# Kernel optimization log

Measured on AMD Instinct MI355X. Metric: run time of the kernel, lower is better.

## Reference

```python
import jax, jax.numpy as jnp
import numpy as np
import math

B, S, H = 4, 1024, 1024
E, TOP_K, WINDOW = 4, 2, 64
CONFIGS = [(8, 'standard'), (12, 'standard'), (8, 'linear'), (8, 'local')]
PARAM_NAMES = ['Wq', 'bq', 'Wk', 'bk', 'Wv', 'bv', 'Wo', 'bo']


def setup_inputs() -> dict:
    key = jax.random.key(0)
    ks = jax.random.split(key, 2 + 8 * E)
    d = {}
    d['x'] = jax.random.normal(ks[0], (B, S, H), jnp.float32)
    d['Wg'] = jax.random.normal(ks[1], (H, E), jnp.float32) * 0.02
    i = 2
    for e, (nh, _) in enumerate(CONFIGS):
        hd = H // nh
        pd = nh * hd  # 1020 for nh=12, else 1024
        shapes = [(H, pd), (pd,), (H, pd), (pd,), (H, pd), (pd,), (pd, H), (H,)]
        for nm, shp in zip(PARAM_NAMES, shapes):
            d[f'e{e}_{nm}'] = jax.random.normal(ks[i], shp, jnp.float32) * 0.02
            i += 1
    d['attention_mask'] = jnp.ones((B, S), jnp.int32)
    return d


def _heads(y, nh, hd):
    b, s, _ = y.shape
    return y.reshape(b, s, nh, hd).transpose(0, 2, 1, 3)  # [b, nh, s, hd]


def _attention_expert(x, mask, Wq, bq, Wk, bk, Wv, bv, Wo, bo, nh, atype):
    b, s, _ = x.shape
    hd = Wq.shape[1] // nh
    scale = math.sqrt(hd)
    q = _heads(x @ Wq + bq, nh, hd)
    k = _heads(x @ Wk + bk, nh, hd)
    v = _heads(x @ Wv + bv, nh, hd)
    if atype == 'linear':
        # kernel-trick linear attention; original ignores attention_mask here
        q = jax.nn.elu(q) + 1.0
        k = jax.nn.elu(k) + 1.0
        kv = jnp.einsum('bhsd,bhse->bhde', k, v)
        num = jnp.einsum('bhqd,bhde->bhqe', q, kv)
        den = jnp.einsum('bhqd,bhd->bhq', q, k.sum(axis=2)) + 1e-6
        out = num / den[..., None]
    else:
        scores = jnp.einsum('bhqd,bhkd->bhqk', q, k) / scale
        if atype == 'local':
            idx = jnp.arange(s)
            dist = idx[None, :] - idx[:, None]  # j - i
            local_mask = jnp.abs(dist) <= WINDOW // 2
            scores = jnp.where(local_mask[None, None], scores, -jnp.inf)
        scores = jnp.where(mask[:, None, None, :] == 0, -jnp.inf, scores)
        probs = jax.nn.softmax(scores, axis=-1)
        probs = jnp.where(jnp.isnan(probs), 0.0, probs)  # nan_to_num(nan=0)
        out = jnp.einsum('bhqk,bhkd->bhqd', probs, v)
    out = out.transpose(0, 2, 1, 3).reshape(b, s, -1)
    return out @ Wo + bo


def _forward(x, Wg, eparams, attention_mask):
    b, s, h = x.shape
    # TopKGating (eval mode: no noise). logits -> top_k -> softmax over selected
    logits = x.reshape(-1, h) @ Wg  # [b*s, E]
    top_vals, top_idx = jax.lax.top_k(logits, TOP_K)
    gate_w = jax.nn.softmax(top_vals, axis=-1).reshape(b, s, TOP_K)
    sel = top_idx.reshape(b, s, TOP_K)
    outs = jnp.stack([
        _attention_expert(x, attention_mask, *eparams[e], CONFIGS[e][0], CONFIGS[e][1])
        for e in range(E)
    ], axis=0)  # [E, b, s, h]
    perm = outs.transpose(1, 2, 0, 3)  # [b, s, E, h]
    selected = jnp.take_along_axis(perm, sel[..., None], axis=2)  # [b, s, K, h]
    return (selected * gate_w[..., None]).sum(axis=2)


def reference(x, Wg,
              e0_Wq, e0_bq, e0_Wk, e0_bk, e0_Wv, e0_bv, e0_Wo, e0_bo,
              e1_Wq, e1_bq, e1_Wk, e1_bk, e1_Wv, e1_bv, e1_Wo, e1_bo,
              e2_Wq, e2_bq, e2_Wk, e2_bk, e2_Wv, e2_bv, e2_Wo, e2_bo,
              e3_Wq, e3_bq, e3_Wk, e3_bk, e3_Wv, e3_bv, e3_Wo, e3_bo,
              attention_mask):
    eparams = [
        (e0_Wq, e0_bq, e0_Wk, e0_bk, e0_Wv, e0_bv, e0_Wo, e0_bo),
        (e1_Wq, e1_bq, e1_Wk, e1_bk, e1_Wv, e1_bv, e1_Wo, e1_bo),
        (e2_Wq, e2_bq, e2_Wk, e2_bk, e2_Wv, e2_bv, e2_Wo, e2_bo),
        (e3_Wq, e3_bq, e3_Wk, e3_bk, e3_Wv, e3_bv, e3_Wo, e3_bo),
    ]
    return _forward(x, Wg, eparams, attention_mask)
```

## Files before the change

kernel.cpp:

```cpp
#include <hip/hip_runtime.h>
#include <cmath>

#define B_ 4
#define S_ 1024
#define H_ 1024

typedef short bf16x8 __attribute__((ext_vector_type(8)));
typedef float f32x4 __attribute__((ext_vector_type(4)));
typedef _Float16 half4 __attribute__((ext_vector_type(4)));

__device__ __forceinline__ unsigned short f2bf(float f) {
  unsigned u = __float_as_uint(f);
  u += 0x7fff + ((u >> 16) & 1);
  return (unsigned short)(u >> 16);
}
__device__ __forceinline__ float bf2f(unsigned short h) {
  return __uint_as_float(((unsigned)h) << 16);
}
__device__ __forceinline__ void gld16(const void* g, void* l) {
  __builtin_amdgcn_global_load_lds(
      (const __attribute__((address_space(1))) unsigned int*)g,
      (__attribute__((address_space(3))) unsigned int*)l, 16, 0, 0);
}

__global__ __launch_bounds__(64) void gate_kernel(
    const float* __restrict__ x, const float* __restrict__ Wg,
    float* __restrict__ gw) {
  int t = blockIdx.x;
  int lane = threadIdx.x;
  const float* xr = x + (size_t)t * H_;
  float a0 = 0.f, a1 = 0.f, a2 = 0.f, a3 = 0.f;
  for (int h = lane; h < H_; h += 64) {
    float xv = xr[h];
    const float* wr = Wg + h * 4;
    a0 += xv * wr[0]; a1 += xv * wr[1]; a2 += xv * wr[2]; a3 += xv * wr[3];
  }
  for (int off = 32; off > 0; off >>= 1) {
    a0 += __shfl_down(a0, off);
    a1 += __shfl_down(a1, off);
    a2 += __shfl_down(a2, off);
    a3 += __shfl_down(a3, off);
  }
  if (lane == 0) {
    float v[4] = {a0, a1, a2, a3};
    int i0 = 0; float b0 = v[0];
    for (int e = 1; e < 4; ++e) if (v[e] > b0) { b0 = v[e]; i0 = e; }
    int i1 = -1; float b1 = -INFINITY;
    for (int e = 0; e < 4; ++e) { if (e == i0) continue; if (v[e] > b1) { b1 = v[e]; i1 = e; } }
    float e1v = expf(b1 - b0);
    float w0 = 1.f / (1.f + e1v);
    float w1 = e1v / (1.f + e1v);
    float o[4] = {0.f, 0.f, 0.f, 0.f};
    o[i0] = w0; o[i1] = w1;
    float* g = gw + t * 4;
    g[0] = o[0]; g[1] = o[1]; g[2] = o[2]; g[3] = o[3];
  }
}

__global__ __launch_bounds__(64) void gate_conv_kernel(
    const float* __restrict__ x, const float* __restrict__ Wg,
    float* __restrict__ gw, unsigned short* __restrict__ xb) {
  int t = blockIdx.x;
  int lane = threadIdx.x;
  const float* xr = x + (size_t)t * H_;
  unsigned short* xbr = xb + (size_t)t * H_;
  float a0 = 0.f, a1 = 0.f, a2 = 0.f, a3 = 0.f;
  for (int h = lane; h < H_; h += 64) {
    float xv = xr[h];
    xbr[h] = f2bf(xv);
    const float* wr = Wg + h * 4;
    a0 += xv * wr[0]; a1 += xv * wr[1]; a2 += xv * wr[2]; a3 += xv * wr[3];
  }
  for (int off = 32; off > 0; off >>= 1) {
    a0 += __shfl_down(a0, off);
    a1 += __shfl_down(a1, off);
    a2 += __shfl_down(a2, off);
    a3 += __shfl_down(a3, off);
  }
  if (lane == 0) {
    float v[4] = {a0, a1, a2, a3};
    int i0 = 0; float b0 = v[0];
    for (int e = 1; e < 4; ++e) if (v[e] > b0) { b0 = v[e]; i0 = e; }
    int i1 = -1; float b1 = -INFINITY;
    for (int e = 0; e < 4; ++e) { if (e == i0) continue; if (v[e] > b1) { b1 = v[e]; i1 = e; } }
    float e1v = expf(b1 - b0);
    float w0 = 1.f / (1.f + e1v);
    float w1 = e1v / (1.f + e1v);
    float o[4] = {0.f, 0.f, 0.f, 0.f};
    o[i0] = w0; o[i1] = w1;
    float* g = gw + t * 4;
    g[0] = o[0]; g[1] = o[1]; g[2] = o[2]; g[3] = o[3];
  }
}

__global__ __launch_bounds__(256) void conv_kernel(
    const float* __restrict__ src, unsigned short* __restrict__ dst,
    int nsrc, int ldsrc) {
  int idx = blockIdx.x * 256 + threadIdx.x;
  int m = idx >> 10, c = idx & 1023;
  dst[idx] = (c < nsrc) ? f2bf(src[(size_t)m * ldsrc + c]) : (unsigned short)0;
}

__global__ __launch_bounds__(256) void wtrans4_kernel(
    const float* __restrict__ s0, const float* __restrict__ s1,
    const float* __restrict__ s2, const float* __restrict__ s3,
    unsigned short* __restrict__ d0, unsigned short* __restrict__ d1,
    unsigned short* __restrict__ d2, unsigned short* __restrict__ d3, int pd) {
  __shared__ float tile[32][33];
  int z = blockIdx.z;
  const float* src = (z == 0) ? s0 : (z == 1) ? s1 : (z == 2) ? s2 : s3;
  unsigned short* dst = (z == 0) ? d0 : (z == 1) ? d1 : (z == 2) ? d2 : d3;
  int ksrc = (z < 3) ? 1024 : pd;
  int nsrc = (z < 3) ? pd : 1024;
  int ldsrc = (z < 3) ? pd : 1024;
  int k0 = blockIdx.x * 32, n0 = blockIdx.y * 32;
  int tx = threadIdx.x & 31, ty = threadIdx.x >> 5;
  for (int i = 0; i < 32; i += 8) {
    int k = k0 + ty + i, n = n0 + tx;
    tile[ty + i][tx] = (k < ksrc && n < nsrc) ? src[(size_t)k * ldsrc + n] : 0.f;
  }
  __syncthreads();
  for (int i = 0; i < 32; i += 8) {
    int n = n0 + ty + i, k = k0 + tx;
    dst[(size_t)n * 1024 + k] = f2bf(tile[tx][ty + i]);
  }
}

struct W16 {
  const float* src[16];
  unsigned short* dst[16];
  int pd[4];
};
__global__ __launch_bounds__(256) void wtrans16_kernel(W16 p) {
  __shared__ float tile[32][33];
  int z = blockIdx.z;
  int e = z >> 2, m = z & 3;
  const float* src = p.src[z];
  unsigned short* dst = p.dst[z];
  int pd = p.pd[e];
  int ksrc = (m < 3) ? 1024 : pd;
  int nsrc = (m < 3) ? pd : 1024;
  int ldsrc = (m < 3) ? pd : 1024;
  int k0 = blockIdx.x * 32, n0 = blockIdx.y * 32;
  int tx = threadIdx.x & 31, ty = threadIdx.x >> 5;
  for (int i = 0; i < 32; i += 8) {
    int k = k0 + ty + i, n = n0 + tx;
    tile[ty + i][tx] = (k < ksrc && n < nsrc) ? src[(size_t)k * ldsrc + n] : 0.f;
  }
  __syncthreads();
  for (int i = 0; i < 32; i += 8) {
    int n = n0 + ty + i, k = k0 + tx;
    dst[(size_t)n * 1024 + k] = f2bf(tile[tx][ty + i]);
  }
}

__global__ __launch_bounds__(256) void gemm_mfma(
    const unsigned short* __restrict__ A, const unsigned short* __restrict__ Bt,
    const float* __restrict__ b0, const float* __restrict__ b1,
    const float* __restrict__ b2, void* __restrict__ Cv, int ldc,
    int nact, int elu_ncut, int out_bf16, int mode,
    const float* __restrict__ gw, int expert, int remap,
    int qs_ncut, float qscale) {
  constexpr int K = 1024;
  __shared__ __align__(16) unsigned short As[128 * 32];
  __shared__ __align__(16) unsigned short Bs[128 * 32];
  int tid = threadIdx.x, wave = tid >> 6, lane = tid & 63;
  int quad = lane >> 4, lrow = lane & 15;
  int rw = (wave >> 1) * 64, cw = (wave & 1) * 64;
  int m0 = blockIdx.y * 128, n0 = blockIdx.x * 128;
  int srow = wave * 32 + (lane >> 2);
  int scol = (lane & 3) * 8;
  const unsigned short* gA = A + (size_t)(m0 + srow) * K + scol;
  const unsigned short* gB = Bt + (size_t)(n0 + srow) * K + scol;
  unsigned short* lA = &As[wave * 1024];
  unsigned short* lB = &Bs[wave * 1024];
  f32x4 acc[4][4];
#pragma unroll
  for (int mt = 0; mt < 4; ++mt)
#pragma unroll
    for (int nt = 0; nt < 4; ++nt) acc[mt][nt] = (f32x4){0.f, 0.f, 0.f, 0.f};

  for (int k0 = 0; k0 < K; k0 += 32) {
    gld16(gA + k0, lA);
    gld16(gA + 16 * K + k0, lA + 512);
    gld16(gB + k0, lB);
    gld16(gB + 16 * K + k0, lB + 512);
    __syncthreads();
    bf16x8 af[4], bfr[4];
#pragma unroll
    for (int t = 0; t < 4; ++t) {
      af[t]  = *(const bf16x8*)&As[(rw + t * 16 + lrow) * 32 + quad * 8];
      bfr[t] = *(const bf16x8*)&Bs[(cw + t * 16 + lrow) * 32 + quad * 8];
    }
#pragma unroll
    for (int mt = 0; mt < 4; ++mt)
#pragma unroll
      for (int nt = 0; nt < 4; ++nt)
        acc[mt][nt] = __builtin_amdgcn_mfma_f32_16x16x32_bf16(
            af[mt], bfr[nt], acc[mt][nt], 0, 0, 0);
    __syncthreads();
  }
#pragma unroll
  for (int nt = 0; nt < 4; ++nt) {
    int n = n0 + cw + nt * 16 + lrow;
    int slice = n >> 10, noff = n & 1023;
    if (noff >= nact) continue;
    const float* bp = (slice == 0) ? b0 : (slice == 1) ? b1 : b2;
    float bias = bp[noff];
    bool do_elu = n < elu_ncut;
    bool do_qs = n < qs_ncut;
    int col = n;
    if (remap) {
      int head = (noff * 12337) >> 20;
      col = slice * 1152 + head * 96 + (noff - head * 85);
    }
#pragma unroll
    for (int mt = 0; mt < 4; ++mt) {
      int mb = m0 + rw + mt * 16 + quad * 4;
#pragma unroll
      for (int r = 0; r < 4; ++r) {
        int m = mb + r;
        float val = acc[mt][nt][r] + bias;
        if (do_elu) val = (val > 0.f) ? val + 1.f : expf(val);
        if (do_qs) val *= qscale;
        size_t ci = (size_t)m * ldc + col;
        if (out_bf16) {
          ((unsigned short*)Cv)[ci] = f2bf(val);
        } else {
          float* C = (float*)Cv;
          if (mode == 0) C[ci] = val;
          else {
            float g = gw[m * 4 + expert];
            if (mode == 1) C[ci] = g * val;
            else           C[ci] += g * val;
          }
        }
      }
    }
  }
}

__device__ __forceinline__ void stage_half(
    const unsigned short* __restrict__ G, int grow0, int kbase,
    unsigned short* lhalf, int wave, int lane) {
#pragma unroll
  for (int j = 0; j < 2; ++j) {
    int t = j * 512 + wave * 64 + lane;
    int rl = t >> 3;
    int cs = (t & 7) * 8;
    int c0 = cs ^ (((rl >> 2) & 1) << 4);
    gld16(G + (size_t)(grow0 + rl) * 1024 + kbase + c0,
          lhalf + (size_t)(j * 512 + wave * 64) * 8);
  }
}

__device__ __forceinline__ void gemm256_core(
    const unsigned short* __restrict__ A, const unsigned short* __restrict__ Bt,
    int m0, int n0, unsigned short* As, unsigned short* Bs,
    f32x4 (&acc)[8][4]) {
  int tid = threadIdx.x;
  int wave = tid >> 6, lane = tid & 63;
  int quad = lane >> 4, l15 = lane & 15;
  int wr = wave >> 2, wc = wave & 3;
#pragma unroll
  for (int mr = 0; mr < 8; ++mr)
#pragma unroll
    for (int nr = 0; nr < 4; ++nr) acc[mr][nr] = (f32x4){0.f, 0.f, 0.f, 0.f};
  stage_half(A, m0, 0, As, wave, lane);
  stage_half(A, m0 + 128, 0, As + 8192, wave, lane);
  stage_half(Bt, n0, 0, Bs, wave, lane);
  stage_half(Bt, n0 + 128, 0, Bs + 8192, wave, lane);
  __syncthreads();
  int cur = 0;
  for (int t = 0; t < 16; ++t) {
    const unsigned short* Ar = As + cur * 16384;
    const unsigned short* Br = Bs + cur * 16384;
    unsigned short* Awr = As + (cur ^ 1) * 16384;
    unsigned short* Bwr = Bs + (cur ^ 1) * 16384;
    int kb = (t + 1) * 64;
    bool more = (t + 1 < 16);
    bf16x8 bfr[4];
#pragma unroll
    for (int p = 0; p < 4; ++p) {
      const int ks = p >> 1, mh = (p & 1) * 4;
      bf16x8 af[4];
#pragma unroll
      for (int i = 0; i < 4; ++i) {
        int row = wr * 128 + (mh + i) * 16 + l15;
        int c = ks * 32 + quad * 8;
        af[i] = *(const bf16x8*)&Ar[row * 64 + (c ^ (((row >> 2) & 1) << 4))];
      }
      if ((p & 1) == 0) {
#pragma unroll
        for (int i = 0; i < 4; ++i) {
          int row = wc * 64 + i * 16 + l15;
          int c = ks * 32 + quad * 8;
          bfr[i] = *(const bf16x8*)&Br[row * 64 + (c ^ (((row >> 2) & 1) << 4))];
        }
      }
      if (more) {
        if (p == 0) stage_half(A, m0, kb, Awr, wave, lane);
        else if (p == 1) stage_half(A, m0 + 128, kb, Awr + 8192, wave, lane);
        else if (p == 2) stage_half(Bt, n0, kb, Bwr, wave, lane);
        else stage_half(Bt, n0 + 128, kb, Bwr + 8192, wave, lane);
      }
      __builtin_amdgcn_s_barrier();
      __builtin_amdgcn_s_setprio(1);
#pragma unroll
      for (int i = 0; i < 4; ++i)
#pragma unroll
        for (int jn = 0; jn < 4; ++jn)
          acc[mh + i][jn] = __builtin_amdgcn_mfma_f32_16x16x32_bf16(
              af[i], bfr[jn], acc[mh + i][jn], 0, 0, 0);
      __builtin_amdgcn_s_setprio(0);
      __builtin_amdgcn_s_barrier();
    }
    __syncthreads();
    cur ^= 1;
  }
}

struct QkvP {
  const unsigned short* Bt[4];
  const float* bq[4];
  const float* bk[4];
  const float* bv[4];
  unsigned short* C[4];
  int ldc[4];
  int nact[4];
  int elu_ncut[4];
  int remap[4];
  int qs_ncut[4];
  float qscale[4];
};
__global__ __launch_bounds__(512, 1) void gemm_qkv4_v2(
    const unsigned short* __restrict__ A, QkvP p) {
  __shared__ __align__(16) unsigned short As[2 * 256 * 64];
  __shared__ __align__(16) unsigned short Bs[2 * 256 * 64];
  int e = blockIdx.z;
  int flat = blockIdx.y * 12 + blockIdx.x;
  int swz = (flat & 7) * 24 + (flat >> 3);
  int m0 = (swz / 12) * 256, n0 = (swz % 12) * 256;
  f32x4 acc[8][4];
  gemm256_core(A, p.Bt[e], m0, n0, As, Bs, acc);
  int nact = p.nact[e], elu_ncut = p.elu_ncut[e], remap = p.remap[e];
  int qs_ncut = p.qs_ncut[e], ldc = p.ldc[e];
  float qscale = p.qscale[e];
  unsigned short* Cv = p.C[e];
  int tid = threadIdx.x, wave = tid >> 6, lane = tid & 63;
  int quad = lane >> 4, l15 = lane & 15;
  int wr = wave >> 2, wc = wave & 3;
#pragma unroll
  for (int nr = 0; nr < 4; ++nr) {
    int n = n0 + wc * 64 + nr * 16 + l15;
    int slice = n >> 10, noff = n & 1023;
    if (noff >= nact) continue;
    const float* bp = (slice == 0) ? p.bq[e] : (slice == 1) ? p.bk[e] : p.bv[e];
    float bias = bp[noff];
    bool do_elu = n < elu_ncut;
    bool do_qs = n < qs_ncut;
    int col = n;
    if (remap) {
      int head = (noff * 12337) >> 20;
      col = slice * 1152 + head * 96 + (noff - head * 85);
    }
#pragma unroll
    for (int mr = 0; mr < 8; ++mr) {
      int mb = m0 + wr * 128 + mr * 16 + quad * 4;
#pragma unroll
      for (int r = 0; r < 4; ++r) {
        int m = mb + r;
        float val = acc[mr][nr][r] + bias;
        if (do_elu) val = (val > 0.f) ? val + 1.f : expf(val);
        if (do_qs) val *= qscale;
        Cv[(size_t)m * ldc + col] = f2bf(val);
      }
    }
  }
}

struct OutP {
  const unsigned short* A[4];
  const unsigned short* B[4];
  const float* bias[4];
};
__global__ __launch_bounds__(512, 1) void gemm_out4_v2(
    OutP p, const float* __restrict__ gw, float* __restrict__ part) {
  __shared__ __align__(16) unsigned short As[2 * 256 * 64];
  __shared__ __align__(16) unsigned short Bs[2 * 256 * 64];
  int e = blockIdx.z;
  int flat = blockIdx.y * 4 + blockIdx.x;
  int swz = (flat & 7) * 8 + (flat >> 3);
  int m0 = (swz / 4) * 256, n0 = (swz % 4) * 256;
  f32x4 acc[8][4];
  gemm256_core(p.A[e], p.B[e], m0, n0, As, Bs, acc);
  const float* bp = p.bias[e];
  float* C = part + (size_t)e * (4096ull * 1024ull);
  int tid = threadIdx.x, wave = tid >> 6, lane = tid & 63;
  int quad = lane >> 4, l15 = lane & 15;
  int wr = wave >> 2, wc = wave & 3;
#pragma unroll
  for (int nr = 0; nr < 4; ++nr) {
    int n = n0 + wc * 64 + nr * 16 + l15;
    float bias = bp[n];
#pragma unroll
    for (int mr = 0; mr < 8; ++mr) {
      int mb = m0 + wr * 128 + mr * 16 + quad * 4;
#pragma unroll
      for (int r = 0; r < 4; ++r) {
        int m = mb + r;
        float g = gw[m * 4 + e];
        C[(size_t)m * 1024 + n] = g * (acc[mr][nr][r] + bias);
      }
    }
  }
}

__global__ __launch_bounds__(256) void reduce4(
    const float* __restrict__ part, float* __restrict__ out) {
  constexpr size_t N = 4096ull * 1024ull;
  size_t idx = ((size_t)blockIdx.x * 256 + threadIdx.x) * 4;
  f32x4 a0 = *(const f32x4*)(part + idx);
  f32x4 a1 = *(const f32x4*)(part + idx + N);
  f32x4 a2 = *(const f32x4*)(part + idx + 2 * N);
  f32x4 a3 = *(const f32x4*)(part + idx + 3 * N);
  f32x4 s;
#pragma unroll
  for (int j = 0; j < 4; ++j) {
    float t = a0[j];
    t += a1[j]; t += a2[j]; t += a3[j];
    s[j] = t;
  }
  *(f32x4*)(out + idx) = s;
}

__global__ __launch_bounds__(256) void padzero(
    unsigned short* __restrict__ qkv1, unsigned short* __restrict__ aob1) {
  int idx = blockIdx.x * 256 + threadIdx.x;
  int m = idx / 396, r = idx % 396;
  int slice = r / 132, r2 = r % 132;
  int head = r2 / 11, c = 85 + r2 % 11;
  qkv1[(size_t)m * 3456 + slice * 1152 + head * 96 + c] = 0;
  if (idx < 4096 * 4) {
    int mm = idx >> 2, cc = 1020 + (idx & 3);
    aob1[(size_t)mm * 1024 + cc] = 0;
  }
}

template <int HD, bool LOCAL>
__device__ __forceinline__ void attn_body(
    char* smem,
    const unsigned short* __restrict__ q, const unsigned short* __restrict__ k,
    const unsigned short* __restrict__ v, const int* __restrict__ amask,
    unsigned short* __restrict__ ao, int ldq, int h) {
  constexpr int HDP = (HD + 31) & ~31;
  constexpr int DCH = HDP / 32;
  constexpr int NDT = HDP / 16;
  constexpr int NCH = HDP / 8;
  constexpr int QT = 256, KT = 64;
  constexpr int KLD = HDP + 8;
  constexpr int VLD = KT + 4;
  constexpr int W2 = 32;
  constexpr int KSZ = KT * KLD;
  constexpr int VSZ = HDP * VLD;
  unsigned short* Ks = (unsigned short*)smem;
  _Float16* Vt = (_Float16*)(smem + 2 * KSZ * 2);
  unsigned long long* amq =
      (unsigned long long*)(smem + 2 * KSZ * 2 + 2 * VSZ * 2);
  int tid = threadIdx.x, wave = tid >> 6, lane = tid & 63;
  int quad = lane >> 4, l15 = lane & 15;
  int q0 = blockIdx.x * QT, b = blockIdx.z;
  size_t baseq = ((size_t)b * S_) * ldq + (size_t)h * HDP;
  size_t baseo = ((size_t)b * S_) * H_ + (size_t)h * HD;

  {
    unsigned long long bb0 = __ballot(amask[b * S_ + wave * 128 + lane] != 0);
    unsigned long long bb1 = __ballot(amask[b * S_ + wave * 128 + 64 + lane] != 0);
    if (lane == 0) { amq[wave * 2] = bb0; amq[wave * 2 + 1] = bb1; }
  }

  int qrow[2];
  bf16x8 qf[2][DCH];
#pragma unroll
  for (int g = 0; g < 2; ++g) {
    qrow[g] = q0 + wave * 32 + g * 16 + l15;
#pragma unroll
    for (int c = 0; c < DCH; ++c)
#pragma unroll
      for (int j = 0; j < 8; ++j) {
        int d = c * 32 + quad * 8 + j;
        qf[g][c][j] =
            (d < HD) ? (short)q[baseq + (size_t)qrow[g] * ldq + d] : (short)0;
      }
  }

  int jlo = 0, jhi = S_;
  if (LOCAL) {
    jlo = q0 - W2; if (jlo < 0) jlo = 0; jlo &= ~(KT - 1);
    jhi = q0 + QT + W2; if (jhi > S_) jhi = S_;
  }

  int skey = tid & 63, sc8a = tid >> 6, sc8b = 8 + (tid >> 6);
  bool sactb = sc8b < NCH;
  const unsigned short* kg = k + baseq + (size_t)skey * ldq;
  const unsigned short* vg = v + baseq + (size_t)skey * ldq;
  bf16x8 kra = {}, krb = {}, vra = {}, vrb = {};
  {
    size_t o = (size_t)jlo * ldq;
    kra = *(const bf16x8*)(kg + o + sc8a * 8);
    vra = *(const bf16x8*)(vg + o + sc8a * 8);
    if (sactb) {
      krb = *(const bf16x8*)(kg + o + sc8b * 8);
      vrb = *(const bf16x8*)(vg + o + sc8b * 8);
    }
  }

  {
    *(bf16x8*)&Ks[skey * KLD + sc8a * 8] = kra;
#pragma unroll
    for (int j = 0; j < 8; ++j)
      Vt[(sc8a * 8 + j) * VLD + skey] = (_Float16)bf2f((unsigned short)vra[j]);
    if (sactb) {
      *(bf16x8*)&Ks[skey * KLD + sc8b * 8] = krb;
#pragma unroll
      for (int j = 0; j < 8; ++j)
        Vt[(sc8b * 8 + j) * VLD + skey] = (_Float16)bf2f((unsigned short)vrb[j]);
    }
  }
  int cur = 0;
  __syncthreads();

  float m_run[2] = {-1e30f, -1e30f}, l_run[2] = {0.f, 0.f};
  f32x4 accd[2][NDT];
#pragma unroll
  for (int g = 0; g < 2; ++g)
#pragma unroll
    for (int dt = 0; dt < NDT; ++dt) accd[g][dt] = (f32x4){0.f, 0.f, 0.f, 0.f};

  for (int j0 = jlo; j0 < jhi; j0 += KT) {
    int jn = j0 + KT;
    if (jn < jhi) {
      size_t o = (size_t)jn * ldq;
      kra = *(const bf16x8*)(kg + o + sc8a * 8);
      vra = *(const bf16x8*)(vg + o + sc8a * 8);
      if (sactb) {
        krb = *(const bf16x8*)(kg + o + sc8b * 8);
        vrb = *(const bf16x8*)(vg + o + sc8b * 8);
      }
    }
    const unsigned short* KsR = Ks + cur * KSZ;
    const _Float16* VtR = Vt + cur * VSZ;
    f32x4 sf[2][4];
#pragma unroll
    for (int kt = 0; kt < 4; ++kt) {
      sf[0][kt] = (f32x4){0.f, 0.f, 0.f, 0.f};
      sf[1][kt] = (f32x4){0.f, 0.f, 0.f, 0.f};
#pragma unroll
      for (int c = 0; c < DCH; ++c) {
        bf16x8 kf = *(const bf16x8*)&KsR[(kt * 16 + l15) * KLD + c * 32 + quad * 8];
        sf[0][kt] = __builtin_amdgcn_mfma_f32_16x16x32_bf16(kf, qf[0][c], sf[0][kt], 0, 0, 0);
        sf[1][kt] = __builtin_amdgcn_mfma_f32_16x16x32_bf16(kf, qf[1][c], sf[1][kt], 0, 0, 0);
      }
    }
    unsigned long long mb = amq[j0 >> 6];
    unsigned mw[2] = {(unsigned)mb, (unsigned)(mb >> 32)};
    float pvv[2][4][4];
    float mx[2] = {-1e30f, -1e30f};
#pragma unroll
    for (int kt = 0; kt < 4; ++kt) {
      unsigned word = mw[kt >> 1];
      int sh = (kt & 1) * 16 + quad * 4;
#pragma unroll
      for (int r = 0; r < 4; ++r) {
        bool okm = (word >> (sh + r)) & 1;
#pragma unroll
        for (int g = 0; g < 2; ++g) {
          bool ok = okm;
          if (LOCAL) {
            int dj = (j0 + kt * 16 + quad * 4 + r) - qrow[g];
            ok = ok && (dj <= W2) && (dj >= -W2);
          }
          float s = ok ? sf[g][kt][r] : -1e30f;
          pvv[g][kt][r] = s;
          mx[g] = fmaxf(mx[g], s);
        }
      }
    }
    half4 pf[2][4];
    float aR[2][4];
#pragma unroll
    for (int g = 0; g < 2; ++g) {
      float mxg = fmaxf(mx[g], __shfl_xor(mx[g], 16));
      mxg = fmaxf(mxg, __shfl_xor(mxg, 32));
      float m_new = fmaxf(m_run[g], mxg);
      float psum = 0.f;
#pragma unroll
      for (int kt = 0; kt < 4; ++kt)
#pragma unroll
        for (int r = 0; r < 4; ++r) {
          float s = pvv[g][kt][r];
          float p = (s > -1e29f) ? __builtin_amdgcn_exp2f(s - m_new) : 0.f;
          pvv[g][kt][r] = p;
          psum += p;
        }
      psum += __shfl_xor(psum, 16);
      psum += __shfl_xor(psum, 32);
      float alpha = __builtin_amdgcn_exp2f(m_run[g] - m_new);
      m_run[g] = m_new;
      l_run[g] = l_run[g] * alpha + psum;
#pragma unroll
      for (int r = 0; r < 4; ++r)
        aR[g][r] = __shfl(alpha, (lane & 48) | (quad * 4 + r));
#pragma unroll
      for (int dt = 0; dt < NDT; ++dt)
#pragma unroll
        for (int r = 0; r < 4; ++r) accd[g][dt][r] *= aR[g][r];
#pragma unroll
      for (int kt = 0; kt < 4; ++kt)
#pragma unroll
        for (int r = 0; r < 4; ++r) pf[g][kt][r] = (_Float16)pvv[g][kt][r];
    }
    if (jn < jhi) {
      unsigned short* KsW = Ks + (cur ^ 1) * KSZ;
      _Float16* VtW = Vt + (cur ^ 1) * VSZ;
      *(bf16x8*)&KsW[skey * KLD + sc8a * 8] = kra;
#pragma unroll
      for (int j = 0; j < 8; ++j)
        VtW[(sc8a * 8 + j) * VLD + skey] = (_Float16)bf2f((unsigned short)vra[j]);
      if (sactb) {
        *(bf16x8*)&KsW[skey * KLD + sc8b * 8] = krb;
#pragma unroll
        for (int j = 0; j < 8; ++j)
          VtW[(sc8b * 8 + j) * VLD + skey] = (_Float16)bf2f((unsigned short)vrb[j]);
      }
    }
#pragma unroll
    for (int dt = 0; dt < NDT; ++dt)
#pragma unroll
      for (int kt = 0; kt < 4; ++kt) {
        half4 vf = *(const half4*)&VtR[(dt * 16 + l15) * VLD + kt * 16 + quad * 4];
        accd[0][dt] = __builtin_amdgcn_mfma_f32_16x16x16f16(pf[0][kt], vf, accd[0][dt], 0, 0, 0);
        accd[1][dt] = __builtin_amdgcn_mfma_f32_16x16x16f16(pf[1][kt], vf, accd[1][dt], 0, 0, 0);
      }
    __syncthreads();
    cur ^= 1;
  }
#pragma unroll
  for (int g = 0; g < 2; ++g) {
    float linv = (l_run[g] > 0.f) ? 1.f / l_run[g] : 0.f;
    float lR[4];
#pragma unroll
    for (int r = 0; r < 4; ++r)
      lR[r] = __shfl(linv, (lane & 48) | (quad * 4 + r));
#pragma unroll
    for (int dt = 0; dt < NDT; ++dt) {
      int d = dt * 16 + l15;
      if (d >= HD) continue;
#pragma unroll
      for (int r = 0; r < 4; ++r) {
        int row = q0 + wave * 32 + g * 16 + quad * 4 + r;
        ao[baseo + (size_t)row * H_ + d] = f2bf(accd[g][dt][r] * lR[r]);
      }
    }
  }
}

template <int HD, bool LOCAL>
__global__ __launch_bounds__(512) void attn_mfma3(
    const unsigned short* __restrict__ q, const unsigned short* __restrict__ k,
    const unsigned short* __restrict__ v, const int* __restrict__ amask,
    unsigned short* __restrict__ ao, int ldq) {
  constexpr int HDP = (HD + 31) & ~31;
  __shared__ __align__(16) char smem[2 * 64 * (HDP + 8) * 2 + 2 * HDP * 68 * 2 + 128];
  attn_body<HD, LOCAL>(smem, q, k, v, amask, ao, ldq, blockIdx.y);
}

#define NSPLIT 4
__device__ __forceinline__ void linkv_body(
    char* smemi, const unsigned short* __restrict__ k,
    const unsigned short* __restrict__ v, float* __restrict__ kvp,
    float* __restrict__ ksump, int ld, int h, int b, int split, int tid) {
  constexpr int HD = 128;
  constexpr int TLD = 34;
  unsigned short* Kt = (unsigned short*)smemi;
  unsigned short* Vt = Kt + HD * TLD;
  int bh = b * 8 + h;
  int wave = tid >> 6, lane = tid & 63;
  int quad = lane >> 4, l15 = lane & 15;
  int rw = (wave >> 1) * 64, cw = (wave & 1) * 64;
  size_t base = ((size_t)b * S_) * ld + (size_t)h * HD;
  int s_begin = split * (S_ / NSPLIT);

  f32x4 acc[4][4];
#pragma unroll
  for (int mt = 0; mt < 4; ++mt)
#pragma unroll
    for (int nt = 0; nt < 4; ++nt) acc[mt][nt] = (f32x4){0.f, 0.f, 0.f, 0.f};
  float ksacc = 0.f;
  int myd = tid & 127, half = tid >> 7;

  for (int c0 = 0; c0 < S_ / NSPLIT; c0 += 32) {
    for (int idx = tid; idx < 32 * HD; idx += 256) {
      int d = idx & 127, s = idx >> 7;
      size_t g = base + (size_t)(s_begin + c0 + s) * ld + d;
      Kt[d * TLD + s] = k[g];
      Vt[d * TLD + s] = v[g];
    }
    __syncthreads();
    bf16x8 af[4], bf[4];
#pragma unroll
    for (int t = 0; t < 4; ++t) {
      af[t] = *(const bf16x8*)&Vt[(rw + t * 16 + l15) * TLD + quad * 8];
      bf[t] = *(const bf16x8*)&Kt[(cw + t * 16 + l15) * TLD + quad * 8];
    }
#pragma unroll
    for (int mt = 0; mt < 4; ++mt)
#pragma unroll
      for (int nt = 0; nt < 4; ++nt)
        acc[mt][nt] = __builtin_amdgcn_mfma_f32_16x16x32_bf16(
            af[mt], bf[nt], acc[mt][nt], 0, 0, 0);
#pragma unroll
    for (int s = 0; s < 16; ++s)
      ksacc += bf2f(Kt[myd * TLD + half * 16 + s]);
    __syncthreads();
  }
  float* red = (float*)Kt;
  if (half == 1) red[myd] = ksacc;
  __syncthreads();
  if (half == 0)
    ksump[((size_t)split * 32 + bh) * HD + myd] = ksacc + red[myd];
  float* kvo = kvp + ((size_t)split * 32 + bh) * (HD * HD);
#pragma unroll
  for (int mt = 0; mt < 4; ++mt)
#pragma unroll
    for (int nt = 0; nt < 4; ++nt) {
      int dk = cw + nt * 16 + l15;
#pragma unroll
      for (int r = 0; r < 4; ++r) {
        int dv = rw + mt * 16 + quad * 4 + r;
        kvo[(size_t)dv * HD + dk] = acc[mt][nt][r];
      }
    }
}

__global__ __launch_bounds__(256) void linkv_mfma(
    const unsigned short* __restrict__ k, const unsigned short* __restrict__ v,
    float* __restrict__ kvp, float* __restrict__ ksump, int ld) {
  __shared__ __align__(16) char smemi[17408];
  linkv_body(smemi, k, v, kvp, ksump, ld, blockIdx.x, blockIdx.y, blockIdx.z,
             threadIdx.x);
}

__global__ __launch_bounds__(512) void attn_mega(
    const unsigned short* __restrict__ qkv0,
    const unsigned short* __restrict__ qkv1,
    const unsigned short* __restrict__ qkv2,
    const unsigned short* __restrict__ qkv3, const int* __restrict__ amask,
    unsigned short* __restrict__ ao0, unsigned short* __restrict__ ao1,
    unsigned short* __restrict__ ao3,
    float* __restrict__ kvp, float* __restrict__ ksump) {
  __shared__ __align__(16) char smem[69760];
  int y = blockIdx.y;
  if (y < 8)
    attn_body<128, false>(smem, qkv0, qkv0 + 1024, qkv0 + 2048, amask, ao0,
                          3072, y);
  else if (y < 20)
    attn_body<85, false>(smem, qkv1, qkv1 + 1152, qkv1 + 2304, amask, ao1,
                         3456, y - 8);
  else if (y < 28)
    attn_body<128, true>(smem, qkv3, qkv3 + 1024, qkv3 + 2048, amask, ao3,
                         3072, y - 20);
  else {
    int sub = threadIdx.x >> 8, stid = threadIdx.x & 255;
    int idx = (y - 28) * 8 + blockIdx.x * 2 + sub;
    linkv_body(smem + sub * 17408, qkv2 + 1024, qkv2 + 2048, kvp, ksump, 3072,
               idx & 7, blockIdx.z, idx >> 3, stid);
  }
}

__global__ __launch_bounds__(256) void linkv_reduce(
    const float* __restrict__ kvp, const float* __restrict__ ksump,
    unsigned short* __restrict__ kvb, float* __restrict__ ksum) {
  int idx = blockIdx.x * 256 + threadIdx.x;
  float s = 0.f;
#pragma unroll
  for (int p = 0; p < NSPLIT; ++p) s += kvp[(size_t)p * (32 * 128 * 128) + idx];
  kvb[idx] = f2bf(s);
  if (idx < 32 * 128) {
    float t = 0.f;
#pragma unroll
    for (int p = 0; p < NSPLIT; ++p) t += ksump[(size_t)p * (32 * 128) + idx];
    ksum[idx] = t;
  }
}

__global__ __launch_bounds__(256) void linattn_mfma(
    const unsigned short* __restrict__ q, const unsigned short* __restrict__ kvT,
    const float* __restrict__ ksum, unsigned short* __restrict__ ao, int ldq) {
  constexpr int KLD = 136;
  __shared__ __align__(16) unsigned short Ks[128 * KLD];
  __shared__ float ksL[128];
  int tid = threadIdx.x, wave = tid >> 6, lane = tid & 63;
  int quad = lane >> 4, l15 = lane & 15;
  int rw = (wave >> 1) * 64, cw = (wave & 1) * 64;
  int q0 = blockIdx.x * 128, h = blockIdx.y, b = blockIdx.z;
  int bh = b * 8 + h;
  size_t baseq = ((size_t)b * S_) * ldq + (size_t)h * 128;
  size_t baseo = ((size_t)b * S_) * H_ + (size_t)h * 128;
  const unsigned short* kvg = kvT + (size_t)bh * (128 * 128);
  for (int idx = tid; idx < 128 * 16; idx += 256) {
    int e = idx >> 4, c = idx & 15;
    *(bf16x8*)&Ks[e * KLD + c * 8] = *(const bf16x8*)&kvg[e * 128 + c * 8];
  }
  if (tid < 128) ksL[tid] = ksum[(size_t)bh * 128 + tid];
  bf16x8 qf[4][4];
#pragma unroll
  for (int mt = 0; mt < 4; ++mt) {
    const unsigned short* qr = q + baseq + (size_t)(q0 + rw + mt * 16 + l15) * ldq;
#pragma unroll
    for (int kc = 0; kc < 4; ++kc)
      qf[mt][kc] = *(const bf16x8*)&qr[kc * 32 + quad * 8];
  }
  __syncthreads();
  f32x4 acc[4][4];
#pragma unroll
  for (int mt = 0; mt < 4; ++mt)
#pragma unroll
    for (int nt = 0; nt < 4; ++nt) acc[mt][nt] = (f32x4){0.f, 0.f, 0.f, 0.f};
#pragma unroll
  for (int kc = 0; kc < 4; ++kc) {
    bf16x8 bf[4];
#pragma unroll
    for (int nt = 0; nt < 4; ++nt)
      bf[nt] = *(const bf16x8*)&Ks[(cw + nt * 16 + l15) * KLD + kc * 32 + quad * 8];
#pragma unroll
    for (int mt = 0; mt < 4; ++mt)
#pragma unroll
      for (int nt = 0; nt < 4; ++nt)
        acc[mt][nt] = __builtin_amdgcn_mfma_f32_16x16x32_bf16(
            qf[mt][kc], bf[nt], acc[mt][nt], 0, 0, 0);
  }
  float den[4];
#pragma unroll
  for (int mt = 0; mt < 4; ++mt) {
    float s = 0.f;
#pragma unroll
    for (int kc = 0; kc < 4; ++kc)
#pragma unroll
      for (int j = 0; j < 8; ++j)
        s += bf2f((unsigned short)qf[mt][kc][j]) * ksL[kc * 32 + quad * 8 + j];
    s += __shfl_xor(s, 16);
    s += __shfl_xor(s, 32);
    den[mt] = s;
  }
#pragma unroll
  for (int mt = 0; mt < 4; ++mt)
#pragma unroll
    for (int r = 0; r < 4; ++r) {
      float dv = __shfl(den[mt], (lane & 48) | (quad * 4 + r));
      float inv = 1.f / (dv + 1e-6f);
      int row = q0 + rw + mt * 16 + quad * 4 + r;
#pragma unroll
      for (int nt = 0; nt < 4; ++nt) {
        int col = cw + nt * 16 + l15;
        ao[baseo + (size_t)row * H_ + col] = f2bf(acc[mt][nt][r] * inv);
      }
    }
}

extern "C" void kernel_launch(void* const* d_in, const int* in_sizes, int n_in,
                              void* d_out, int out_size, void* d_ws, size_t ws_size,
                              hipStream_t stream) {
  const float* x = (const float*)d_in[0];
  const float* Wg = (const float*)d_in[1];
  const int* amask = (const int*)d_in[34];
  float* out = (float*)d_out;
  char* ws = (char*)d_ws;
  const size_t MiB = 1ull << 20;
  const int nhs[4] = {8, 12, 8, 8};
  const float LOG2E = 1.4426950408889634f;

  if (ws_size >= 157 * MiB) {
    float* gw = (float*)ws;
    float* ksum = (float*)(ws + (64ull << 10));
    unsigned short* kvb = (unsigned short*)(ws + 1 * MiB);
    unsigned short* xb = (unsigned short*)(ws + 4 * MiB);
    float* kvp = (float*)(ws + 4 * MiB);
    float* ksump = (float*)(ws + 12 * MiB);
    unsigned short* woT[4];
    for (int e = 0; e < 4; ++e)
      woT[e] = (unsigned short*)(ws + (18 + 2 * e) * MiB);
    const size_t qkvOff[4] = {26 * MiB, 50 * MiB, 77 * MiB, 101 * MiB};
    unsigned short* qkvE[4];
    for (int e = 0; e < 4; ++e) qkvE[e] = (unsigned short*)(ws + qkvOff[e]);
    float* part = (float*)(ws + 26 * MiB);
    unsigned short* aobE[4];
    for (int e = 0; e < 4; ++e)
      aobE[e] = (unsigned short*)(ws + (125 + 8 * e) * MiB);
    unsigned short* qkvT4 = (unsigned short*)(ws + 125 * MiB);

    gate_conv_kernel<<<4096, 64, 0, stream>>>(x, Wg, gw, xb);

    W16 w;
    for (int e = 0; e < 4; ++e) {
      w.pd[e] = nhs[e] * (H_ / nhs[e]);
      for (int m = 0; m < 3; ++m) {
        w.src[e * 4 + m] = (const float*)d_in[2 + 8 * e + 2 * m];
        w.dst[e * 4 + m] = qkvT4 + (size_t)(e * 3 + m) * (1 << 20);
      }
      w.src[e * 4 + 3] = (const float*)d_in[2 + 8 * e + 6];
      w.dst[e * 4 + 3] = woT[e];
    }
    wtrans16_kernel<<<dim3(32, 32, 16), 256, 0, stream>>>(w);

    QkvP qp;
    for (int e = 0; e < 4; ++e) {
      int hd = H_ / nhs[e];
      int pd = nhs[e] * hd;
      qp.Bt[e] = qkvT4 + (size_t)(e * 3) * (1 << 20);
      qp.bq[e] = (const float*)d_in[2 + 8 * e + 1];
      qp.bk[e] = (const float*)d_in[2 + 8 * e + 3];
      qp.bv[e] = (const float*)d_in[2 + 8 * e + 5];
      qp.C[e] = qkvE[e];
      qp.ldc[e] = (e == 1) ? 3456 : 3072;
      qp.nact[e] = (pd == 1020) ? 1020 : 1024;
      qp.elu_ncut[e] = (e == 2) ? 2048 : 0;
      qp.remap[e] = (e == 1) ? 1 : 0;
      qp.qs_ncut[e] = (e == 2) ? 0 : 1024;
      qp.qscale[e] = LOG2E / sqrtf((float)hd);
    }
    gemm_qkv4_v2<<<dim3(12, 16, 4), 512, 0, stream>>>(xb, qp);

    padzero<<<6336, 256, 0, stream>>>(qkvE[1], aobE[1]);

    attn_mega<<<dim3(S_ / 256, 32, B_), 512, 0, stream>>>(
        qkvE[0], qkvE[1], qkvE[2], qkvE[3], amask, aobE[0], aobE[1], aobE[3],
        kvp, ksump);

    linkv_reduce<<<(32 * 128 * 128) / 256, 256, 0, stream>>>(kvp, ksump, kvb, ksum);
    linattn_mfma<<<dim3(S_ / 128, 8, B_), 256, 0, stream>>>(
        qkvE[2], kvb, ksum, aobE[2], 3072);

    OutP p;
    for (int e = 0; e < 4; ++e) {
      p.A[e] = aobE[e];
      p.B[e] = woT[e];
      p.bias[e] = (const float*)d_in[2 + 8 * e + 7];
    }
    gemm_out4_v2<<<dim3(4, 16, 4), 512, 0, stream>>>(p, gw, part);
    reduce4<<<4096, 256, 0, stream>>>(part, out);
    return;
  }

  float* gw            = (float*)(ws + 0);
  unsigned short* kvb  = (unsigned short*)(ws + (1ull << 20));
  float* ksum          = (float*)(ws + (3ull << 20) + (1ull << 19));
  unsigned short* xb   = (unsigned short*)(ws + (4ull << 20));
  unsigned short* qkvT = (unsigned short*)(ws + (12ull << 20));
  unsigned short* woT  = (unsigned short*)(ws + (18ull << 20));
  unsigned short* qkv  = (unsigned short*)(ws + (20ull << 20));
  unsigned short* aob  = (unsigned short*)(ws + (49ull << 20));
  float* kvp           = (float*)(ws + (57ull << 20));
  float* ksump         = (float*)(ws + (73ull << 20));

  conv_kernel<<<16384, 256, 0, stream>>>(x, xb, 1024, 1024);
  gate_kernel<<<4096, 64, 0, stream>>>(x, Wg, gw);

  for (int e = 0; e < 4; ++e) {
    const float* Wq = (const float*)d_in[2 + 8 * e + 0];
    const float* bq = (const float*)d_in[2 + 8 * e + 1];
    const float* Wk = (const float*)d_in[2 + 8 * e + 2];
    const float* bk = (const float*)d_in[2 + 8 * e + 3];
    const float* Wv = (const float*)d_in[2 + 8 * e + 4];
    const float* bv = (const float*)d_in[2 + 8 * e + 5];
    const float* Wo = (const float*)d_in[2 + 8 * e + 6];
    const float* bo = (const float*)d_in[2 + 8 * e + 7];
    int nh = nhs[e];
    int hd = H_ / nh;
    int pd = nh * hd;
    int ldqkv = (e == 1) ? 3456 : 3072;
    int qs_ncut = (e == 2) ? 0 : 1024;
    float qscale = LOG2E / sqrtf((float)hd);

    wtrans4_kernel<<<dim3(32, 32, 4), 256, 0, stream>>>(
        Wq, Wk, Wv, Wo, qkvT, qkvT + (1 << 20), qkvT + (2 << 20), woT, pd);

    gemm_mfma<<<dim3(24, 32), 256, 0, stream>>>(
        xb, qkvT, bq, bk, bv, qkv, ldqkv,
        (pd == 1020) ? 1020 : 1024, (e == 2) ? 2048 : 0, 1, 0, nullptr, 0,
        (e == 1) ? 1 : 0, qs_ncut, qscale);

    if (e == 2) {
      const unsigned short* qb = qkv;
      const unsigned short* kb = qkv + 1024;
      const unsigned short* vb = qkv + 2048;
      linkv_mfma<<<dim3(8, B_, NSPLIT), 256, 0, stream>>>(kb, vb, kvp, ksump, 3072);
      linkv_reduce<<<(32 * 128 * 128) / 256, 256, 0, stream>>>(kvp, ksump, kvb, ksum);
      linattn_mfma<<<dim3(S_ / 128, 8, B_), 256, 0, stream>>>(qb, kvb, ksum, aob, 3072);
    } else if (e == 1) {
      attn_mfma3<85, false><<<dim3(S_ / 256, 12, B_), 512, 0, stream>>>(
          qkv, qkv + 1152, qkv + 2304, amask, aob, 3456);
    } else if (e == 3) {
      attn_mfma3<128, true><<<dim3(S_ / 256, 8, B_), 512, 0, stream>>>(
          qkv, qkv + 1024, qkv + 2048, amask, aob, 3072);
    } else {
      attn_mfma3<128, false><<<dim3(S_ / 256, 8, B_), 512, 0, stream>>>(
          qkv, qkv + 1024, qkv + 2048, amask, aob, 3072);
    }

    gemm_mfma<<<dim3(8, 32), 256, 0, stream>>>(
        aob, woT, bo, bo, bo, out, 1024, 1024, 0, 0, (e == 0) ? 1 : 2, gw, e, 0,
        0, 1.0f);
  }
}
```

Before: 524.6 us.

## Restructure 256x256 GEMM mainloop with full-tile prefetch and wider LDS swizzle

Replaces the four-phase interleaved mainloop with one that issues the whole next K-tile's global-to-LDS loads at the start of each iteration. It then runs two k-substeps, each loading 8 A and 4 B fragments before 32 MFMAs. The per-phase s_barriers are dropped in favour of a sched_barrier, and the LDS swizzle changes from a 1-bit XOR on bit 4 to a 3-bit XOR of row&7 into the column. The aim is fewer barriers and fewer LDS bank conflicts. The cost is higher register pressure from holding 8 A fragments, and a less finely interleaved load/compute schedule.

```diff
diff --git a/kernel.cpp b/kernel.cpp
--- a/kernel.cpp
+++ b/kernel.cpp
@@ -240,17 +240,20 @@
   }
 }
 
-__device__ __forceinline__ void stage_half(
-    const unsigned short* __restrict__ G, int grow0, int kbase,
-    unsigned short* lhalf, int wave, int lane) {
+__device__ __forceinline__ void stage_tile(
+    const unsigned short* __restrict__ A, const unsigned short* __restrict__ Bt,
+    int m0, int n0, int kbase, unsigned short* Abuf, unsigned short* Bbuf,
+    int wave, int lane) {
 #pragma unroll
   for (int j = 0; j < 2; ++j) {
     int t = j * 512 + wave * 64 + lane;
     int rl = t >> 3;
-    int cs = (t & 7) * 8;
-    int c0 = cs ^ (((rl >> 2) & 1) << 4);
-    gld16(G + (size_t)(grow0 + rl) * 1024 + kbase + c0,
-          lhalf + (size_t)(j * 512 + wave * 64) * 8);
+    int c0 = ((t & 7) * 8) ^ ((rl & 7) << 3);
+    int ldst = (j * 512 + wave * 64) * 8;
+    gld16(A + (size_t)(m0 + rl) * 1024 + kbase + c0, Abuf + ldst);
+    gld16(A + (size_t)(m0 + 128 + rl) * 1024 + kbase + c0, Abuf + 8192 + ldst);
+    gld16(Bt + (size_t)(n0 + rl) * 1024 + kbase + c0, Bbuf + ldst);
+    gld16(Bt + (size_t)(n0 + 128 + rl) * 1024 + kbase + c0, Bbuf + 8192 + ldst);
   }
 }
 
@@ -266,54 +269,38 @@
   for (int mr = 0; mr < 8; ++mr)
 #pragma unroll
     for (int nr = 0; nr < 4; ++nr) acc[mr][nr] = (f32x4){0.f, 0.f, 0.f, 0.f};
-  stage_half(A, m0, 0, As, wave, lane);
-  stage_half(A, m0 + 128, 0, As + 8192, wave, lane);
-  stage_half(Bt, n0, 0, Bs, wave, lane);
-  stage_half(Bt, n0 + 128, 0, Bs + 8192, wave, lane);
+  stage_tile(A, Bt, m0, n0, 0, As, Bs, wave, lane);
   __syncthreads();
   int cur = 0;
   for (int t = 0; t < 16; ++t) {
+    if (t + 1 < 16)
+      stage_tile(A, Bt, m0, n0, (t + 1) * 64, As + (cur ^ 1) * 16384,
+                 Bs + (cur ^ 1) * 16384, wave, lane);
     const unsigned short* Ar = As + cur * 16384;
     const unsigned short* Br = Bs + cur * 16384;
-    unsigned short* Awr = As + (cur ^ 1) * 16384;
-    unsigned short* Bwr = Bs + (cur ^ 1) * 16384;
-    int kb = (t + 1) * 64;
-    bool more = (t + 1 < 16);
-    bf16x8 bfr[4];
-#pragma unroll
-    for (int p = 0; p < 4; ++p) {
-      const int ks = p >> 1, mh = (p & 1) * 4;
-      bf16x8 af[4];
+#pragma unroll
+    for (int ks = 0; ks < 2; ++ks) {
+      int c = ks * 32 + quad * 8;
+      bf16x8 af[8], bfr[4];
+#pragma unroll
+      for (int i = 0; i < 8; ++i) {
+        int row = wr * 128 + i * 16 + l15;
+        af[i] = *(const bf16x8*)&Ar[row * 64 + (c ^ ((row & 7) << 3))];
+      }
 #pragma unroll
       for (int i = 0; i < 4; ++i) {
-        int row = wr * 128 + (mh + i) * 16 + l15;
-        int c = ks * 32 + quad * 8;
-        af[i] = *(const bf16x8*)&Ar[row * 64 + (c ^ (((row >> 2) & 1) << 4))];
-      }
-      if ((p & 1) == 0) {
-#pragma unroll
-        for (int i = 0; i < 4; ++i) {
-          int row = wc * 64 + i * 16 + l15;
-          int c = ks * 32 + quad * 8;
-          bfr[i] = *(const bf16x8*)&Br[row * 64 + (c ^ (((row >> 2) & 1) << 4))];
-        }
-      }
-      if (more) {
-        if (p == 0) stage_half(A, m0, kb, Awr, wave, lane);
-        else if (p == 1) stage_half(A, m0 + 128, kb, Awr + 8192, wave, lane);
-        else if (p == 2) stage_half(Bt, n0, kb, Bwr, wave, lane);
-        else stage_half(Bt, n0 + 128, kb, Bwr + 8192, wave, lane);
-      }
-      __builtin_amdgcn_s_barrier();
+        int row = wc * 64 + i * 16 + l15;
+        bfr[i] = *(const bf16x8*)&Br[row * 64 + (c ^ ((row & 7) << 3))];
+      }
       __builtin_amdgcn_s_setprio(1);
 #pragma unroll
-      for (int i = 0; i < 4; ++i)
-#pragma unroll
-        for (int jn = 0; jn < 4; ++jn)
-          acc[mh + i][jn] = __builtin_amdgcn_mfma_f32_16x16x32_bf16(
-              af[i], bfr[jn], acc[mh + i][jn], 0, 0, 0);
+      for (int mr = 0; mr < 8; ++mr)
+#pragma unroll
+        for (int nr = 0; nr < 4; ++nr)
+          acc[mr][nr] = __builtin_amdgcn_mfma_f32_16x16x32_bf16(
+              af[mr], bfr[nr], acc[mr][nr], 0, 0, 0);
       __builtin_amdgcn_s_setprio(0);
-      __builtin_amdgcn_s_barrier();
+      __builtin_amdgcn_sched_barrier(0);
     }
     __syncthreads();
     cur ^= 1;
```

Result: slower. 561.9 us (+7.1%).
